# Kernel optimization log

Hardware: AMD Instinct MI355X
Metric: run time of the kernel (lower is better)

Reference implementation:

```python
import jax, jax.numpy as jnp
import numpy as np

EPSILON = 1.5  # quality-tolerance threshold from init_kwargs
NEG_INF = -1000000000.0


def setup_inputs() -> dict:
    key = jax.random.key(0)
    k1, k2, k3 = jax.random.split(key, 3)
    B, S, D, E = 4, 4096, 2048, 64
    return {
        "hidden_states": jax.random.normal(k1, (B, S, D), dtype=jnp.float32),
        "gate_W": jax.random.normal(k2, (E, D), dtype=jnp.float32),  # nn.Linear weight [out,in]
        "secret_projection": jax.random.normal(k3, (D, E), dtype=jnp.float32),
        "top_k": 2,
    }


def reference(hidden_states, gate_W, secret_projection, top_k):
    # raw gate logits: Linear without bias -> x @ W^T
    raw_logits = jnp.einsum("bsd,ed->bse", hidden_states, gate_W)
    # watermark bias via secret LSH projection
    watermark_bias = jnp.einsum("bsd,de->bse", hidden_states, secret_projection)
    # indifference zone: experts whose logit is within epsilon of the max
    max_logits = jnp.max(raw_logits, axis=-1, keepdims=True)
    safe_mask = raw_logits >= max_logits - EPSILON
    modified_scores = jnp.where(safe_mask, watermark_bias, jnp.asarray(NEG_INF, raw_logits.dtype))
    # top-k over watermark-preferred safe experts
    _, selected_experts = jax.lax.top_k(modified_scores, top_k)
    # gather original logits at selected experts, softmax over the k slots
    router_logits = jnp.take_along_axis(raw_logits, selected_experts, axis=-1)
    routing_weights = jax.nn.softmax(router_logits, axis=-1)
    return routing_weights, selected_experts
```

## Files before the change

kernel.cpp:

```cpp
#include <hip/hip_runtime.h>
#include <stdint.h>


#define DDIM 2048
#define NEXP 64
#define NEG_INF  -1000000000.0f
#define MRG_RAW  0.04f
#define MRG_WM   0.15f
#define RST      130

typedef __attribute__((ext_vector_type(8))) short bf16x8;
typedef __attribute__((ext_vector_type(4))) float f32x4;

union BFrag { bf16x8 v; uint32_t w[4]; uint4 q; };

__device__ inline void split8_rne(const float* a, bf16x8* hi, bf16x8* lo) {
    BFrag h, l;
    #pragma unroll
    for (int p = 0; p < 4; ++p) {
        const uint32_t u0 = __float_as_uint(a[2*p]);
        const uint32_t u1 = __float_as_uint(a[2*p+1]);
        const uint32_t h0 = (u0 + 0x7FFFu + ((u0 >> 16) & 1u)) >> 16;
        const uint32_t h1 = (u1 + 0x7FFFu + ((u1 >> 16) & 1u)) >> 16;
        const float r0 = a[2*p]   - __uint_as_float(h0 << 16);
        const float r1 = a[2*p+1] - __uint_as_float(h1 << 16);
        const uint32_t v0 = __float_as_uint(r0);
        const uint32_t v1 = __float_as_uint(r1);
        const uint32_t l0 = (v0 + 0x7FFFu + ((v0 >> 16) & 1u)) >> 16;
        const uint32_t l1 = (v1 + 0x7FFFu + ((v1 >> 16) & 1u)) >> 16;
        h.w[p] = h0 | (h1 << 16);
        l.w[p] = l0 | (l1 << 16);
    }
    *hi = h.v; *lo = l.v;
}

__device__ inline void split8t(const float* a, bf16x8* hi, bf16x8* lo) {
    BFrag h, l;
    #pragma unroll
    for (int p = 0; p < 4; ++p) {
        const uint32_t u0 = __float_as_uint(a[2*p]);
        const uint32_t u1 = __float_as_uint(a[2*p+1]);
        h.w[p] = (u0 >> 16) | (u1 & 0xFFFF0000u);
        const float r0 = a[2*p]   - __uint_as_float(u0 & 0xFFFF0000u);
        const float r1 = a[2*p+1] - __uint_as_float(u1 & 0xFFFF0000u);
        l.w[p] = (__float_as_uint(r0) >> 16) | (__float_as_uint(r1) & 0xFFFF0000u);
    }
    *hi = h.v; *lo = l.v;
}

__global__ void prep_b(const float* __restrict__ gateW, const float* __restrict__ secret,
                       uint4* __restrict__ wsB) {
    const int kstep = blockIdx.x;
    const int s = threadIdx.x >> 6;
    const int l = threadIdx.x & 63;
    const int col = s * 16 + (l & 15);
    const int kb  = kstep * 32 + (l >> 4) * 8;
    float v[8];
    if (col < NEXP) {
        #pragma unroll
        for (int j = 0; j < 8; ++j) v[j] = gateW[(size_t)col * DDIM + kb + j];
    } else {
        #pragma unroll
        for (int j = 0; j < 8; ++j) v[j] = secret[(size_t)(kb + j) * NEXP + (col - NEXP)];
    }
    bf16x8 hi, lo; split8_rne(v, &hi, &lo);
    const size_t base = (size_t)(kstep * 8 + s) * 128 + l;
    BFrag t;
    t.v = hi; wsB[base]      = t.q;
    t.v = lo; wsB[base + 64] = t.q;
}

__global__ __launch_bounds__(256, 3)
void gemm32(const float* __restrict__ x, const bf16x8* __restrict__ wsB,
            float* __restrict__ wsL, int ntok)
{
    __shared__ float red[2][16 * RST];

    const int tid = threadIdx.x;
    const int w = tid >> 6;
    const int p = w & 1;
    const int h = w >> 1;
    const int l = tid & 63;
    const int c = l & 15;
    const int g = l >> 4;
    const int rowbase = blockIdx.x * 32 + p * 16;

    f32x4 acc[8];
    #pragma unroll
    for (int s = 0; s < 8; ++s) acc[s] = (f32x4){0.f, 0.f, 0.f, 0.f};

    const float* xr = x + (size_t)(rowbase + c) * DDIM + h * 1024 + g * 8;
    const bf16x8* bp = wsB + ((size_t)h * 32 * 8) * 128 + l;

    for (int ts = 0; ts < 32; ++ts) {
        bf16x8 bq[16];
        #pragma unroll
        for (int s = 0; s < 8; ++s) {
            bq[2*s]     = bp[(size_t)(ts * 8 + s) * 128];
            bq[2*s + 1] = bp[(size_t)(ts * 8 + s) * 128 + 64];
        }
        const float4 a0 = *reinterpret_cast<const float4*>(xr + ts * 32);
        const float4 a1 = *reinterpret_cast<const float4*>(xr + ts * 32 + 4);
        const float va[8] = {a0.x, a0.y, a0.z, a0.w, a1.x, a1.y, a1.z, a1.w};
        bf16x8 ah, al;
        split8t(va, &ah, &al);

        #pragma unroll
        for (int s = 0; s < 8; ++s) {
            acc[s] = __builtin_amdgcn_mfma_f32_16x16x32_bf16(ah, bq[2*s],     acc[s], 0, 0, 0);
            acc[s] = __builtin_amdgcn_mfma_f32_16x16x32_bf16(ah, bq[2*s + 1], acc[s], 0, 0, 0);
            acc[s] = __builtin_amdgcn_mfma_f32_16x16x32_bf16(al, bq[2*s],     acc[s], 0, 0, 0);
        }
    }

    if (h == 1) {
        float* L = red[p];
        #pragma unroll
        for (int s = 0; s < 8; ++s)
            #pragma unroll
            for (int r = 0; r < 4; ++r)
                L[(g * 4 + r) * RST + s * 16 + c] = acc[s][r];
    }
    __syncthreads();
    if (h == 0) {
        const float* L = red[p];
        #pragma unroll
        for (int s = 0; s < 8; ++s)
            #pragma unroll
            for (int r = 0; r < 4; ++r) {
                const float v = acc[s][r] + L[(g * 4 + r) * RST + s * 16 + c];
                wsL[(size_t)(rowbase + g * 4 + r) * 128 + s * 16 + c] = v;
            }
    }
}

__global__ __launch_bounds__(256, 4)
void router_k(const float* __restrict__ wsL,
              const float* __restrict__ x,
              const float* __restrict__ gateW,
              const float* __restrict__ secret,
              float* __restrict__ out, int ntok)
{
    const int t = blockIdx.x * 4 + (threadIdx.x >> 6);
    const int e = threadIdx.x & 63;

    float raw = wsL[(size_t)t * 128 + e];
    float wm  = wsL[(size_t)t * 128 + NEXP + e];

    float rmax = raw;
    #pragma unroll
    for (int off = 32; off; off >>= 1) rmax = fmaxf(rmax, __shfl_xor(rmax, off));

    if (__any(fabsf(raw - (rmax - 1.5f)) < MRG_RAW)) {
        float s0 = 0.f, s1 = 0.f, s2 = 0.f, s3 = 0.f;
        const float4* xr = reinterpret_cast<const float4*>(x + (size_t)t * DDIM);
        const float4* wr = reinterpret_cast<const float4*>(gateW + (size_t)e * DDIM);
        for (int k = 0; k < DDIM / 4; ++k) {
            const float4 a = xr[k], b = wr[k];
            s0 = fmaf(a.x, b.x, s0); s1 = fmaf(a.y, b.y, s1);
            s2 = fmaf(a.z, b.z, s2); s3 = fmaf(a.w, b.w, s3);
        }
        raw = (s0 + s1) + (s2 + s3);
        rmax = raw;
        #pragma unroll
        for (int off = 32; off; off >>= 1) rmax = fmaxf(rmax, __shfl_xor(rmax, off));
    }

    const bool safe = (raw >= rmax - 1.5f);
    float m = safe ? wm : NEG_INF;

    float v1 = m; int e1 = e;
    #pragma unroll
    for (int off = 32; off; off >>= 1) {
        const float ov = __shfl_xor(v1, off); const int oi = __shfl_xor(e1, off);
        if (ov > v1 || (ov == v1 && oi < e1)) { v1 = ov; e1 = oi; }
    }
    float v2 = (e == e1) ? -3.0e38f : m; int e2 = e;
    #pragma unroll
    for (int off = 32; off; off >>= 1) {
        const float ov = __shfl_xor(v2, off); const int oi = __shfl_xor(e2, off);
        if (ov > v2 || (ov == v2 && oi < e2)) { v2 = ov; e2 = oi; }
    }
    float v3 = (e == e1 || e == e2) ? -3.0e38f : m; int e3 = e;
    #pragma unroll
    for (int off = 32; off; off >>= 1) {
        const float ov = __shfl_xor(v3, off); const int oi = __shfl_xor(e3, off);
        if (ov > v3 || (ov == v3 && oi < e3)) { v3 = ov; e3 = oi; }
    }

    const bool wmRisk = (v2 > NEG_INF + 1.0f && v1 - v2 < MRG_WM) ||
                        (v3 > NEG_INF + 1.0f && v2 - v3 < MRG_WM);
    if (__any(wmRisk)) {
        float s0 = 0.f, s1 = 0.f, s2 = 0.f, s3 = 0.f;
        const float* xr = x + (size_t)t * DDIM;
        for (int k = 0; k < DDIM; k += 4) {
            s0 = fmaf(xr[k + 0], secret[(size_t)(k + 0) * NEXP + e], s0);
            s1 = fmaf(xr[k + 1], secret[(size_t)(k + 1) * NEXP + e], s1);
            s2 = fmaf(xr[k + 2], secret[(size_t)(k + 2) * NEXP + e], s2);
            s3 = fmaf(xr[k + 3], secret[(size_t)(k + 3) * NEXP + e], s3);
        }
        m = safe ? ((s0 + s1) + (s2 + s3)) : NEG_INF;
        v1 = m; e1 = e;
        #pragma unroll
        for (int off = 32; off; off >>= 1) {
            const float ov = __shfl_xor(v1, off); const int oi = __shfl_xor(e1, off);
            if (ov > v1 || (ov == v1 && oi < e1)) { v1 = ov; e1 = oi; }
        }
        v2 = (e == e1) ? -3.0e38f : m; e2 = e;
        #pragma unroll
        for (int off = 32; off; off >>= 1) {
            const float ov = __shfl_xor(v2, off); const int oi = __shfl_xor(e2, off);
            if (ov > v2 || (ov == v2 && oi < e2)) { v2 = ov; e2 = oi; }
        }
    }

    const float l1 = __shfl(raw, e1);
    const float l2 = __shfl(raw, e2);

    if (e == 0) {
        const float mm = fmaxf(l1, l2);
        const float x1 = expf(l1 - mm), x2 = expf(l2 - mm);
        const float inv = 1.0f / (x1 + x2);
        out[(size_t)t * 2 + 0] = x1 * inv;
        out[(size_t)t * 2 + 1] = x2 * inv;
        out[(size_t)2 * ntok + t * 2 + 0] = (float)e1;
        out[(size_t)2 * ntok + t * 2 + 1] = (float)e2;
    }
}

extern "C" void kernel_launch(void* const* d_in, const int* in_sizes, int n_in,
                              void* d_out, int out_size, void* d_ws, size_t ws_size,
                              hipStream_t stream) {
    const float* x      = (const float*)d_in[0];
    const float* gateW  = (const float*)d_in[1];
    const float* secret = (const float*)d_in[2];
    float* out = (float*)d_out;

    const int ntok = in_sizes[0] / DDIM;
    uint4* wsB = (uint4*)d_ws;
    float* wsL = (float*)((char*)d_ws + (2u << 20));

    prep_b<<<64, 512, 0, stream>>>(gateW, secret, wsB);
    gemm32<<<ntok / 32, 256, 0, stream>>>(x, (const bf16x8*)wsB, wsL, ntok);
    router_k<<<ntok / 4, 256, 0, stream>>>(wsL, x, gateW, secret, out, ntok);
}
```

Before: 117.2 us.

## Stage B fragments in LDS with double-buffered async loads, drop K-split

Replaces the K-split GEMM, where each wave read its own B fragments from global memory, with a kernel in which four waves each own 16 rows and share B tiles staged in LDS through global_load_lds with double buffering. This lets the four waves reuse each B fragment instead of fetching it separately, and removes the cross-wave LDS reduction. The cost is fewer blocks (ntok/64), one barrier per K-step, and a longer serial K loop per wave with launch bounds of one block per SIMD set.

```diff
diff --git a/kernel.cpp b/kernel.cpp
--- a/kernel.cpp
+++ b/kernel.cpp
@@ -4,10 +4,10 @@
 
 #define DDIM 2048
 #define NEXP 64
+#define NT   64
 #define NEG_INF  -1000000000.0f
 #define MRG_RAW  0.04f
 #define MRG_WM   0.15f
-#define RST      130
 
 typedef __attribute__((ext_vector_type(8))) short bf16x8;
 typedef __attribute__((ext_vector_type(4))) float f32x4;
@@ -70,68 +70,77 @@
     t.v = lo; wsB[base + 64] = t.q;
 }
 
-__global__ __launch_bounds__(256, 3)
-void gemm32(const float* __restrict__ x, const bf16x8* __restrict__ wsB,
-            float* __restrict__ wsL, int ntok)
+__device__ inline void gl_lds16(const char* g, char* l) {
+    __builtin_amdgcn_global_load_lds(
+        (const __attribute__((address_space(1))) void*)g,
+        (__attribute__((address_space(3))) void*)l, 16, 0, 0);
+}
+
+__global__ __launch_bounds__(256, 1)
+void gemm_lds(const float* __restrict__ x, const char* __restrict__ wsB,
+              float* __restrict__ wsL, int ntok)
 {
-    __shared__ float red[2][16 * RST];
+    __shared__ __align__(16) char lds[2][16384];
 
     const int tid = threadIdx.x;
-    const int w = tid >> 6;
-    const int p = w & 1;
-    const int h = w >> 1;
-    const int l = tid & 63;
+    const int w = tid >> 6, l = tid & 63;
     const int c = l & 15;
     const int g = l >> 4;
-    const int rowbase = blockIdx.x * 32 + p * 16;
+    const int rowbase = blockIdx.x * 64 + w * 16;
 
     f32x4 acc[8];
     #pragma unroll
     for (int s = 0; s < 8; ++s) acc[s] = (f32x4){0.f, 0.f, 0.f, 0.f};
 
-    const float* xr = x + (size_t)(rowbase + c) * DDIM + h * 1024 + g * 8;
-    const bf16x8* bp = wsB + ((size_t)h * 32 * 8) * 128 + l;
-
-    for (int ts = 0; ts < 32; ++ts) {
-        bf16x8 bq[16];
-        #pragma unroll
-        for (int s = 0; s < 8; ++s) {
-            bq[2*s]     = bp[(size_t)(ts * 8 + s) * 128];
-            bq[2*s + 1] = bp[(size_t)(ts * 8 + s) * 128 + 64];
-        }
-        const float4 a0 = *reinterpret_cast<const float4*>(xr + ts * 32);
-        const float4 a1 = *reinterpret_cast<const float4*>(xr + ts * 32 + 4);
-        const float va[8] = {a0.x, a0.y, a0.z, a0.w, a1.x, a1.y, a1.z, a1.w};
+    const float* xr = x + (size_t)(rowbase + c) * DDIM + g * 8;
+
+    #define STAGE(ts, buf)                                                        \
+        {                                                                         \
+            _Pragma("unroll")                                                     \
+            for (int j = 0; j < 4; ++j) {                                         \
+                const int f = j * 4 + w;                                          \
+                const int s_ = f >> 1, hl = f & 1;                                \
+                gl_lds16(wsB + ((size_t)((ts) * 8 + s_) * 128 + hl * 64 + l) * 16,\
+                         &lds[buf][f * 1024 + l * 16]);                           \
+            }                                                                     \
+        }
+
+    float4 A0a, A0b, A1a, A1b;
+    STAGE(0, 0);
+    A0a = *reinterpret_cast<const float4*>(xr);
+    A0b = *reinterpret_cast<const float4*>(xr + 4);
+
+    for (int ts = 0; ts < NT; ++ts) {
+        __syncthreads();
+
+        if (ts < NT - 1) {
+            STAGE(ts + 1, (ts + 1) & 1);
+            A1a = *reinterpret_cast<const float4*>(xr + (ts + 1) * 32);
+            A1b = *reinterpret_cast<const float4*>(xr + (ts + 1) * 32 + 4);
+        }
+
+        const float va[8] = {A0a.x, A0a.y, A0a.z, A0a.w, A0b.x, A0b.y, A0b.z, A0b.w};
         bf16x8 ah, al;
         split8t(va, &ah, &al);
 
+        const char* bb = lds[ts & 1];
         #pragma unroll
         for (int s = 0; s < 8; ++s) {
-            acc[s] = __builtin_amdgcn_mfma_f32_16x16x32_bf16(ah, bq[2*s],     acc[s], 0, 0, 0);
-            acc[s] = __builtin_amdgcn_mfma_f32_16x16x32_bf16(ah, bq[2*s + 1], acc[s], 0, 0, 0);
-            acc[s] = __builtin_amdgcn_mfma_f32_16x16x32_bf16(al, bq[2*s],     acc[s], 0, 0, 0);
-        }
-    }
-
-    if (h == 1) {
-        float* L = red[p];
-        #pragma unroll
-        for (int s = 0; s < 8; ++s)
-            #pragma unroll
-            for (int r = 0; r < 4; ++r)
-                L[(g * 4 + r) * RST + s * 16 + c] = acc[s][r];
-    }
-    __syncthreads();
-    if (h == 0) {
-        const float* L = red[p];
-        #pragma unroll
-        for (int s = 0; s < 8; ++s)
-            #pragma unroll
-            for (int r = 0; r < 4; ++r) {
-                const float v = acc[s][r] + L[(g * 4 + r) * RST + s * 16 + c];
-                wsL[(size_t)(rowbase + g * 4 + r) * 128 + s * 16 + c] = v;
-            }
-    }
+            const bf16x8 bh = *reinterpret_cast<const bf16x8*>(bb + (2*s)     * 1024 + l * 16);
+            const bf16x8 bl = *reinterpret_cast<const bf16x8*>(bb + (2*s + 1) * 1024 + l * 16);
+            acc[s] = __builtin_amdgcn_mfma_f32_16x16x32_bf16(ah, bh, acc[s], 0, 0, 0);
+            acc[s] = __builtin_amdgcn_mfma_f32_16x16x32_bf16(ah, bl, acc[s], 0, 0, 0);
+            acc[s] = __builtin_amdgcn_mfma_f32_16x16x32_bf16(al, bh, acc[s], 0, 0, 0);
+        }
+        A0a = A1a; A0b = A1b;
+    }
+    #undef STAGE
+
+    #pragma unroll
+    for (int s = 0; s < 8; ++s)
+        #pragma unroll
+        for (int r = 0; r < 4; ++r)
+            wsL[(size_t)(rowbase + g * 4 + r) * 128 + s * 16 + c] = acc[s][r];
 }
 
 __global__ __launch_bounds__(256, 4)
@@ -241,6 +250,6 @@
     float* wsL = (float*)((char*)d_ws + (2u << 20));
 
     prep_b<<<64, 512, 0, stream>>>(gateW, secret, wsB);
-    gemm32<<<ntok / 32, 256, 0, stream>>>(x, (const bf16x8*)wsB, wsL, ntok);
+    gemm_lds<<<ntok / 64, 256, 0, stream>>>(x, (const char*)wsB, wsL, ntok);
     router_k<<<ntok / 4, 256, 0, stream>>>(wsL, x, gateW, secret, out, ntok);
 }
```

New measurement: 111.1 us. -5.2%, faster.

## Restructure router GEMM to 64-row warp tiles with 4-way K-split partials

Applied to the files above, without the earlier changes.

Replaces the 32-row block GEMM, which split K in two and reduced through shared memory, with 256-row blocks where each warp computes a 64-row tile (4 M-fragments) over a quarter of K. The loads are software-pipelined into register arrays. Each K-split writes its partial logits to a workspace slice, and the router kernel sums the four slices. The intent is to reuse each B fragment across four A fragments, cutting B traffic, and to overlap global loads with MFMA. The cost is heavy register pressure (the fully unrolled prefetch arrays may spill), four times the partial-output traffic, and only 64 blocks of work.

```diff
diff --git a/kernel.cpp b/kernel.cpp
--- a/kernel.cpp
+++ b/kernel.cpp
@@ -4,15 +4,16 @@
 
 #define DDIM 2048
 #define NEXP 64
+#define KSPL 4
+#define NTS  16
 #define NEG_INF  -1000000000.0f
 #define MRG_RAW  0.04f
 #define MRG_WM   0.15f
-#define RST      130
 
 typedef __attribute__((ext_vector_type(8))) short bf16x8;
 typedef __attribute__((ext_vector_type(4))) float f32x4;
 
-union BFrag { bf16x8 v; uint32_t w[4]; uint4 q; };
+union BFrag { bf16x8 v; f32x4 f; uint32_t w[4]; uint4 q; };
 
 __device__ inline void split8_rne(const float* a, bf16x8* hi, bf16x8* lo) {
     BFrag h, l;
@@ -70,72 +71,89 @@
     t.v = lo; wsB[base + 64] = t.q;
 }
 
-__global__ __launch_bounds__(256, 3)
-void gemm32(const float* __restrict__ x, const bf16x8* __restrict__ wsB,
-            float* __restrict__ wsL, int ntok)
+__global__ __launch_bounds__(256, 1)
+void gemm_r(const float* __restrict__ x, const uint4* __restrict__ wsB,
+            float* __restrict__ wsP, int ntok)
 {
-    __shared__ float red[2][16 * RST];
-
     const int tid = threadIdx.x;
-    const int w = tid >> 6;
-    const int p = w & 1;
-    const int h = w >> 1;
-    const int l = tid & 63;
+    const int w = tid >> 6, l = tid & 63;
     const int c = l & 15;
     const int g = l >> 4;
-    const int rowbase = blockIdx.x * 32 + p * 16;
-
-    f32x4 acc[8];
-    #pragma unroll
-    for (int s = 0; s < 8; ++s) acc[s] = (f32x4){0.f, 0.f, 0.f, 0.f};
-
-    const float* xr = x + (size_t)(rowbase + c) * DDIM + h * 1024 + g * 8;
-    const bf16x8* bp = wsB + ((size_t)h * 32 * 8) * 128 + l;
-
-    for (int ts = 0; ts < 32; ++ts) {
-        bf16x8 bq[16];
+    const int q  = blockIdx.x & (KSPL - 1);
+    const int mb = blockIdx.x / KSPL;
+    const int wrow = mb * 256 + w * 64;
+
+    f32x4 acc[4][8];
+    #pragma unroll
+    for (int m = 0; m < 4; ++m)
+        #pragma unroll
+        for (int s = 0; s < 8; ++s) acc[m][s] = (f32x4){0.f, 0.f, 0.f, 0.f};
+
+    const float* xr = x + (size_t)(wrow + c) * DDIM + q * (DDIM / KSPL) + g * 8;
+    const uint4* bp = wsB + (size_t)(q * NTS * 8) * 128 + l;
+
+    float4 Aa[NTS + 1][4], Ab[NTS + 1][4];
+    BFrag  BH[NTS + 1][8], BL[NTS + 1][8];
+
+    #pragma unroll
+    for (int m = 0; m < 4; ++m) {
+        const float* xm = xr + (size_t)(m * 16) * DDIM;
+        Aa[0][m] = *reinterpret_cast<const float4*>(xm);
+        Ab[0][m] = *reinterpret_cast<const float4*>(xm + 4);
+    }
+    #pragma unroll
+    for (int s = 0; s < 8; ++s) {
+        BH[0][s].q = bp[(size_t)s * 128];
+        BL[0][s].q = bp[(size_t)s * 128 + 64];
+    }
+
+    #pragma unroll
+    for (int ts = 0; ts < NTS; ++ts) {
+        const int nx = (ts + 1 < NTS) ? ts + 1 : ts;
+        #pragma unroll
+        for (int m = 0; m < 4; ++m) {
+            const float* xm = xr + (size_t)(m * 16) * DDIM + nx * 32;
+            Aa[ts + 1][m] = *reinterpret_cast<const float4*>(xm);
+            Ab[ts + 1][m] = *reinterpret_cast<const float4*>(xm + 4);
+        }
         #pragma unroll
         for (int s = 0; s < 8; ++s) {
-            bq[2*s]     = bp[(size_t)(ts * 8 + s) * 128];
-            bq[2*s + 1] = bp[(size_t)(ts * 8 + s) * 128 + 64];
-        }
-        const float4 a0 = *reinterpret_cast<const float4*>(xr + ts * 32);
-        const float4 a1 = *reinterpret_cast<const float4*>(xr + ts * 32 + 4);
-        const float va[8] = {a0.x, a0.y, a0.z, a0.w, a1.x, a1.y, a1.z, a1.w};
-        bf16x8 ah, al;
-        split8t(va, &ah, &al);
-
-        #pragma unroll
-        for (int s = 0; s < 8; ++s) {
-            acc[s] = __builtin_amdgcn_mfma_f32_16x16x32_bf16(ah, bq[2*s],     acc[s], 0, 0, 0);
-            acc[s] = __builtin_amdgcn_mfma_f32_16x16x32_bf16(ah, bq[2*s + 1], acc[s], 0, 0, 0);
-            acc[s] = __builtin_amdgcn_mfma_f32_16x16x32_bf16(al, bq[2*s],     acc[s], 0, 0, 0);
-        }
-    }
-
-    if (h == 1) {
-        float* L = red[p];
+            BH[ts + 1][s].q = bp[(size_t)(nx * 8 + s) * 128];
+            BL[ts + 1][s].q = bp[(size_t)(nx * 8 + s) * 128 + 64];
+        }
+
+        bf16x8 ah[4], al[4];
+        #pragma unroll
+        for (int m = 0; m < 4; ++m) {
+            const float va[8] = {Aa[ts][m].x, Aa[ts][m].y, Aa[ts][m].z, Aa[ts][m].w,
+                                 Ab[ts][m].x, Ab[ts][m].y, Ab[ts][m].z, Ab[ts][m].w};
+            split8t(va, &ah[m], &al[m]);
+        }
+
+        #pragma unroll
+        for (int s = 0; s < 8; ++s)
+            #pragma unroll
+            for (int m = 0; m < 4; ++m) {
+                acc[m][s] = __builtin_amdgcn_mfma_f32_16x16x32_bf16(ah[m], BH[ts][s].v, acc[m][s], 0, 0, 0);
+                acc[m][s] = __builtin_amdgcn_mfma_f32_16x16x32_bf16(ah[m], BL[ts][s].v, acc[m][s], 0, 0, 0);
+                acc[m][s] = __builtin_amdgcn_mfma_f32_16x16x32_bf16(al[m], BH[ts][s].v, acc[m][s], 0, 0, 0);
+            }
+    }
+
+    const size_t MN = (size_t)ntok * 128;
+    #pragma unroll
+    for (int m = 0; m < 4; ++m)
         #pragma unroll
         for (int s = 0; s < 8; ++s)
             #pragma unroll
             for (int r = 0; r < 4; ++r)
-                L[(g * 4 + r) * RST + s * 16 + c] = acc[s][r];
-    }
-    __syncthreads();
-    if (h == 0) {
-        const float* L = red[p];
-        #pragma unroll
-        for (int s = 0; s < 8; ++s)
-            #pragma unroll
-            for (int r = 0; r < 4; ++r) {
-                const float v = acc[s][r] + L[(g * 4 + r) * RST + s * 16 + c];
-                wsL[(size_t)(rowbase + g * 4 + r) * 128 + s * 16 + c] = v;
-            }
-    }
-}
-
+                wsP[(size_t)q * MN + (size_t)(wrow + m * 16 + g * 4 + r) * 128 + s * 16 + c]
+                    = acc[m][s][r];
+}
+
+template <int KSPLIT>
 __global__ __launch_bounds__(256, 4)
-void router_k(const float* __restrict__ wsL,
+void router_k(const float* __restrict__ wsP,
               const float* __restrict__ x,
               const float* __restrict__ gateW,
               const float* __restrict__ secret,
@@ -143,9 +161,14 @@
 {
     const int t = blockIdx.x * 4 + (threadIdx.x >> 6);
     const int e = threadIdx.x & 63;
-
-    float raw = wsL[(size_t)t * 128 + e];
-    float wm  = wsL[(size_t)t * 128 + NEXP + e];
+    const size_t MN = (size_t)ntok * 128;
+
+    float raw = 0.f, wm = 0.f;
+    #pragma unroll
+    for (int q = 0; q < KSPLIT; ++q) {
+        raw += wsP[(size_t)q * MN + (size_t)t * 128 + e];
+        wm  += wsP[(size_t)q * MN + (size_t)t * 128 + NEXP + e];
+    }
 
     float rmax = raw;
     #pragma unroll
@@ -238,9 +261,9 @@
 
     const int ntok = in_sizes[0] / DDIM;
     uint4* wsB = (uint4*)d_ws;
-    float* wsL = (float*)((char*)d_ws + (2u << 20));
+    float* wsP = (float*)((char*)d_ws + (2u << 20));
 
     prep_b<<<64, 512, 0, stream>>>(gateW, secret, wsB);
-    gemm32<<<ntok / 32, 256, 0, stream>>>(x, (const bf16x8*)wsB, wsL, ntok);
-    router_k<<<ntok / 4, 256, 0, stream>>>(wsL, x, gateW, secret, out, ntok);
-}
+    gemm_r<<<(ntok / 256) * KSPL, 256, 0, stream>>>(x, wsB, wsP, ntok);
+    router_k<KSPL><<<ntok / 4, 256, 0, stream>>>(wsP, x, gateW, secret, out, ntok);
+}
```

Result: slower. 121.5 us (+3.6%).
